# Performance work log

Hardware: AMD Instinct MI355X
Metric: run time of the kernel (lower is better)

Reference implementation:

```python
import jax, jax.numpy as jnp
import numpy as np

N = 20000          # nodes
E = 320000         # edges
G = 256            # g_dim
H1 = 256           # h1_dim (RGCN out)
H2 = 128           # h2_dim (per-head transformer out)
HEADS = 4
R = 8              # num relations
EPS_BN = 1e-5


def setup_inputs() -> dict:
    key = jax.random.key(0)
    ks = jax.random.split(key, 16)
    inp = {
        "node_features": jax.random.normal(ks[0], (N, G), jnp.float32),
        "node_type": jax.random.randint(ks[1], (N,), 0, 3),
        "edge_index": jax.random.randint(ks[2], (2, E), 0, N),
        "edge_type": jax.random.randint(ks[3], (E,), 0, R),
        # RGCNConv params
        "W_rel": jax.random.normal(ks[4], (R, G, H1), jnp.float32) * (1.0 / np.sqrt(G)),
        "W_root": jax.random.normal(ks[5], (G, H1), jnp.float32) * (1.0 / np.sqrt(G)),
        "b_rgcn": jnp.zeros((H1,), jnp.float32),
        # TransformerConv params (concat=True -> HEADS*H2 output)
        "W_q": jax.random.normal(ks[6], (H1, HEADS * H2), jnp.float32) * (1.0 / np.sqrt(H1)),
        "b_q": jnp.zeros((HEADS * H2,), jnp.float32),
        "W_k": jax.random.normal(ks[7], (H1, HEADS * H2), jnp.float32) * (1.0 / np.sqrt(H1)),
        "b_k": jnp.zeros((HEADS * H2,), jnp.float32),
        "W_v": jax.random.normal(ks[8], (H1, HEADS * H2), jnp.float32) * (1.0 / np.sqrt(H1)),
        "b_v": jnp.zeros((HEADS * H2,), jnp.float32),
        "W_skip": jax.random.normal(ks[9], (H1, HEADS * H2), jnp.float32) * (1.0 / np.sqrt(H1)),
        "b_skip": jnp.zeros((HEADS * H2,), jnp.float32),
        # BatchNorm1d params (training-mode batch stats)
        "bn_gamma": jnp.ones((HEADS * H2,), jnp.float32),
        "bn_beta": jnp.zeros((HEADS * H2,), jnp.float32),
    }
    return inp


def reference(node_features, node_type, edge_index, edge_type,
              W_rel, W_root, b_rgcn,
              W_q, b_q, W_k, b_k, W_v, b_v, W_skip, b_skip,
              bn_gamma, bn_beta):
    x = node_features
    src, dst = edge_index[0], edge_index[1]  # messages flow src -> dst

    # ---- RGCNConv (mean aggregation per relation, root weight, bias) ----
    xr = jnp.einsum('nd,rdh->nrh', x, W_rel)           # (N, R, H1)
    msg = xr[src, edge_type]                            # (E, H1)
    seg = dst * R + edge_type                           # combined (node, relation) segment id
    sums = jax.ops.segment_sum(msg, seg, num_segments=N * R)
    cnt = jax.ops.segment_sum(jnp.ones((E,), x.dtype), seg, num_segments=N * R)
    mean = sums / jnp.maximum(cnt, 1.0)[:, None]
    agg = mean.reshape(N, R, H1).sum(axis=1)            # sum over relations
    h1 = agg + x @ W_root + b_rgcn                      # (N, H1)

    # ---- TransformerConv (heads=HEADS, concat=True, root skip) ----
    q = (h1 @ W_q + b_q).reshape(N, HEADS, H2)
    k = (h1 @ W_k + b_k).reshape(N, HEADS, H2)
    v = (h1 @ W_v + b_v).reshape(N, HEADS, H2)

    scale = 1.0 / np.sqrt(H2)
    alpha = jnp.sum(q[dst] * k[src], axis=-1) * scale   # (E, HEADS)
    amax = jax.ops.segment_max(alpha, dst, num_segments=N)  # per-dst softmax max
    ea = jnp.exp(alpha - amax[dst])
    denom = jax.ops.segment_sum(ea, dst, num_segments=N)
    attn = ea / jnp.maximum(denom[dst], 1e-16)          # (E, HEADS)

    out = jax.ops.segment_sum(attn[:, :, None] * v[src], dst, num_segments=N)
    out = out.reshape(N, HEADS * H2) + h1 @ W_skip + b_skip

    # ---- BatchNorm1d (batch stats) + LeakyReLU(0.01) ----
    mu = out.mean(axis=0)
    var = out.var(axis=0)
    xn = (out - mu) * jax.lax.rsqrt(var + EPS_BN)
    y = bn_gamma * xn + bn_beta
    return jax.nn.leaky_relu(y, negative_slope=0.01)
```

## Files before the change

kernel.cpp:

```cpp
#include <hip/hip_runtime.h>

static const int N_NODES = 20000;
static const int N_EDGES = 320000;
static const int GDIM    = 256;
static const int H1DIM   = 256;
static const int C2DIM   = 512;
static const int NREL    = 8;
static const int NSEG    = N_NODES * NREL;

typedef _Float16 __attribute__((ext_vector_type(8))) half8;
typedef _Float16 __attribute__((ext_vector_type(4))) half4;
typedef _Float16 __attribute__((ext_vector_type(2))) half2v;
typedef __attribute__((ext_vector_type(4))) float f32x4;

__device__ __forceinline__ void gload_lds16(const void* g, void* l) {
  __builtin_amdgcn_global_load_lds(
      (const __attribute__((address_space(1))) unsigned int*)g,
      (__attribute__((address_space(3))) unsigned int*)l, 16, 0, 0);
}

__device__ __forceinline__ void swz_bxy(int& bx, int& by) {
  int nx   = gridDim.x;
  int nwg  = nx * gridDim.y;
  int orig = blockIdx.y * nx + blockIdx.x;
  int xcd  = orig & 7;
  int q    = nwg >> 3, r = nwg & 7;
  int base = xcd < r ? xcd * (q + 1) : r * (q + 1) + (xcd - r) * q;
  int wgid = base + (orig >> 3);
  bx = wgid % nx; by = wgid / nx;
}

template<int OUT_HALF>
__global__ __launch_bounds__(256) void gemm_mfma_k(
    const _Float16* __restrict__ A, const _Float16* __restrict__ Bt,
    const float* __restrict__ bias, void* __restrict__ Cout,
    int M, int N, int K)
{
  __shared__ _Float16 As[128 * 64];
  __shared__ _Float16 Bs[128 * 64];
  int bx, by; swz_bxy(bx, by);
  const int tid  = threadIdx.x;
  const int wid  = tid >> 6, lane = tid & 63;
  const int wr   = wid >> 1, wc = wid & 1;
  const int brow = by * 128;
  const int bcol = bx * 128;
  const int l15  = lane & 15, lhi = lane >> 4;
  const int srow = wid * 32;
  const int lrow = lane >> 3;
  const int lchk = lane & 7;

  f32x4 acc[4][4] = {};

  for (int k0 = 0; k0 < K; k0 += 64) {
    __syncthreads();
#pragma unroll
    for (int i = 0; i < 4; ++i) {
      int row = srow + i * 8 + lrow;
      int gc  = lchk ^ (row & 7);
      gload_lds16(A  + (size_t)(brow + row) * K + k0 + gc * 8,
                  &As[(srow + i * 8) * 64]);
      gload_lds16(Bt + (size_t)(bcol + row) * K + k0 + gc * 8,
                  &Bs[(srow + i * 8) * 64]);
    }
    __syncthreads();
#pragma unroll
    for (int kf = 0; kf < 2; ++kf) {
      int cc = kf * 4 + lhi;
      half8 af[4], bfr[4];
#pragma unroll
      for (int mi = 0; mi < 4; ++mi) {
        int row = wr * 64 + mi * 16 + l15;
        af[mi] = ((const half8*)As)[row * 8 + (cc ^ (row & 7))];
      }
#pragma unroll
      for (int ni = 0; ni < 4; ++ni) {
        int row = wc * 64 + ni * 16 + l15;
        bfr[ni] = ((const half8*)Bs)[row * 8 + (cc ^ (row & 7))];
      }
#pragma unroll
      for (int mi = 0; mi < 4; ++mi)
#pragma unroll
        for (int ni = 0; ni < 4; ++ni)
          acc[mi][ni] = __builtin_amdgcn_mfma_f32_16x16x32_f16(
              af[mi], bfr[ni], acc[mi][ni], 0, 0, 0);
    }
  }
#pragma unroll
  for (int ni = 0; ni < 4; ++ni) {
    int col = bcol + wc * 64 + ni * 16 + l15;
    float bb = bias ? bias[col] : 0.f;
#pragma unroll
    for (int mi = 0; mi < 4; ++mi) {
      int row0 = brow + wr * 64 + mi * 16 + lhi * 4;
#pragma unroll
      for (int j = 0; j < 4; ++j) {
        int r = row0 + j;
        if (r >= M) continue;
        float val = acc[mi][ni][j] + bb;
        if (OUT_HALF) ((_Float16*)Cout)[(size_t)r * N + col] = (_Float16)val;
        else          ((float*)Cout)[(size_t)r * N + col] = val;
      }
    }
  }
}

__global__ __launch_bounds__(256) void prep_k(
    const int* __restrict__ dst, const int* __restrict__ et, int* __restrict__ hist,
    const float* __restrict__ W_root, const float* __restrict__ W_rel,
    _Float16* __restrict__ Wt_cat2,
    const float* __restrict__ Wq, const float* __restrict__ Wk,
    const float* __restrict__ Wv, const float* __restrict__ Ws,
    const float* __restrict__ bq, const float* __restrict__ bk,
    const float* __restrict__ bv, const float* __restrict__ bs,
    _Float16* __restrict__ Wt_qk, float* __restrict__ bias_cat,
    const float* __restrict__ x, _Float16* __restrict__ xh)
{
  int b = blockIdx.x, tid = threadIdx.x;
  if (b < 1250) {
    int e = b * 256 + tid;
    if (e < N_EDGES) atomicAdd(&hist[dst[e] * NREL + et[e]], 1);
  } else if (b < 3554) {
    int idx = (b - 1250) * 256 + tid;
    int n2 = idx >> 8, k = idx & 255;
    float v;
    if (n2 < 256) v = W_root[(size_t)k * H1DIM + n2];
    else {
      int rr = (n2 - 256) >> 8, c = (n2 - 256) & 255;
      v = W_rel[((size_t)rr * 256 + k) * 256 + c];
    }
    Wt_cat2[idx] = (_Float16)v;
  } else if (b < 5602) {
    int idx = (b - 3554) * 256 + tid;
    int n = idx >> 8, k = idx & 255;
    int sel = n >> 9, c = n & 511;
    const float* W = sel == 0 ? Wq : sel == 1 ? Wk : sel == 2 ? Wv : Ws;
    Wt_qk[(size_t)n * 256 + k] = (_Float16)W[(size_t)k * C2DIM + c];
    if (k == 0) {
      const float* B = sel == 0 ? bq : sel == 1 ? bk : sel == 2 ? bv : bs;
      bias_cat[n] = B[c];
    }
  } else {
    int i = (b - 5602) * 256 + tid;
    float4 v = ((const float4*)x)[i];
    half4 o = {(_Float16)v.x, (_Float16)v.y, (_Float16)v.z, (_Float16)v.w};
    ((half4*)xh)[i] = o;
  }
}

__global__ __launch_bounds__(1024) void scan_local_k(
    const int* __restrict__ in, int* __restrict__ out, int* __restrict__ bsum, int n)
{
  __shared__ int s[1024];
  int gi = blockIdx.x * 1024 + threadIdx.x;
  int v = gi < n ? in[gi] : 0;
  s[threadIdx.x] = v; __syncthreads();
  for (int off = 1; off < 1024; off <<= 1) {
    int t = threadIdx.x >= off ? s[threadIdx.x - off] : 0;
    __syncthreads();
    s[threadIdx.x] += t;
    __syncthreads();
  }
  if (gi < n) out[gi] = s[threadIdx.x] - v;
  if (threadIdx.x == 1023) bsum[blockIdx.x] = s[1023];
}

__global__ __launch_bounds__(1024) void scan_addoff_k(
    int* __restrict__ off, const int* __restrict__ bsum,
    int* __restrict__ cur, int n, int nb)
{
  __shared__ int s[1024];
  int t = threadIdx.x;
  int v = t < nb ? bsum[t] : 0;
  s[t] = v; __syncthreads();
  for (int o = 1; o < 1024; o <<= 1) {
    int u = t >= o ? s[t - o] : 0;
    __syncthreads();
    s[t] += u;
    __syncthreads();
  }
  int blockOff = blockIdx.x == 0 ? 0 : s[blockIdx.x - 1];
  int gi = blockIdx.x * 1024 + t;
  if (gi < n) {
    int val = off[gi] + blockOff;
    off[gi] = val;
    cur[gi] = val;
  }
  if (gi == 0) off[n] = N_EDGES;
}

__global__ void reorder_k(const int* __restrict__ src, const int* __restrict__ dst,
                          const int* __restrict__ et,
                          int* __restrict__ cur, int* __restrict__ esrc)
{
  int e = blockIdx.x * blockDim.x + threadIdx.x;
  if (e >= N_EDGES) return;
  int seg = dst[e] * NREL + et[e];
  esrc[atomicAdd(&cur[seg], 1)] = src[e];
}

__global__ __launch_bounds__(256) void agg_h1_k(
    const _Float16* __restrict__ Y, const float* __restrict__ b_rgcn,
    const int* __restrict__ off, const int* __restrict__ esrc,
    _Float16* __restrict__ h1h)
{
  int d = blockIdx.x * 4 + (threadIdx.x >> 6);
  if (d >= N_NODES) return;
  int lane = threadIdx.x & 63;
  half4 rt = ((const half4*)(Y + (size_t)d * 2304))[lane];
  float4 bb = ((const float4*)b_rgcn)[lane];
  float4 acc = make_float4((float)rt.x + bb.x, (float)rt.y + bb.y,
                           (float)rt.z + bb.z, (float)rt.w + bb.w);
  for (int r = 0; r < NREL; ++r) {
    int seg = d * NREL + r;
    int beg = off[seg], end = off[seg + 1];
    if (beg >= end) continue;
    float4 a2 = make_float4(0.f, 0.f, 0.f, 0.f);
    for (int e = beg; e < end; ++e) {
      int s = esrc[e];
      half4 v = ((const half4*)(Y + (size_t)s * 2304 + 256 + r * 256))[lane];
      a2.x += (float)v.x; a2.y += (float)v.y;
      a2.z += (float)v.z; a2.w += (float)v.w;
    }
    float inv = 1.0f / (float)(end - beg);
    acc.x += a2.x * inv; acc.y += a2.y * inv;
    acc.z += a2.z * inv; acc.w += a2.w * inv;
  }
  half4 o = {(_Float16)acc.x, (_Float16)acc.y, (_Float16)acc.z, (_Float16)acc.w};
  ((half4*)(h1h + (size_t)d * 256))[lane] = o;
}

__global__ __launch_bounds__(256) void attn_fused_k(
    const _Float16* __restrict__ qkvs,
    const int* __restrict__ off, const int* __restrict__ esrc,
    _Float16* __restrict__ outh)
{
  int d = blockIdx.x * 4 + (threadIdx.x >> 6);
  if (d >= N_NODES) return;
  int lane = threadIdx.x & 63;
  half8 qr = ((const half8*)(qkvs + (size_t)d * 2048))[lane];
  float qf[8];
#pragma unroll
  for (int j = 0; j < 8; ++j) qf[j] = (float)qr[j];
  float m = -3.4e38f, ssum = 0.f;
  float av[8] = {};
  int beg = off[d * NREL], end = off[d * NREL + NREL];
  half8 krN = {}, vrN = {};
  if (beg < end) {
    int s0 = esrc[beg];
    const half8* row = (const half8*)(qkvs + (size_t)s0 * 2048 + 512);
    krN = row[lane];
    vrN = row[64 + lane];
  }
  for (int e = beg; e < end; ++e) {
    half8 kr = krN, vr = vrN;
    if (e + 1 < end) {
      int s1 = esrc[e + 1];
      const half8* row = (const half8*)(qkvs + (size_t)s1 * 2048 + 512);
      krN = row[lane];
      vrN = row[64 + lane];
    }
    float p = 0.f;
#pragma unroll
    for (int j = 0; j < 8; ++j) p += qf[j] * (float)kr[j];
    p += __shfl_xor(p, 1); p += __shfl_xor(p, 2);
    p += __shfl_xor(p, 4); p += __shfl_xor(p, 8);
    float a = p * 0.08838834764831845f;
    float mn = fmaxf(m, a);
    float corr = __expf(m - mn), w = __expf(a - mn);
    ssum = ssum * corr + w;
#pragma unroll
    for (int j = 0; j < 8; ++j) av[j] = av[j] * corr + w * (float)vr[j];
    m = mn;
  }
  float inv = 1.0f / fmaxf(ssum, 1e-16f);
  half8 sr = ((const half8*)(qkvs + (size_t)d * 2048 + 1536))[lane];
  half8 o;
#pragma unroll
  for (int j = 0; j < 8; ++j) o[j] = (_Float16)(av[j] * inv + (float)sr[j]);
  ((half8*)(outh + (size_t)d * C2DIM))[lane] = o;
}

__global__ __launch_bounds__(256) void bn_stats_k(
    const _Float16* __restrict__ x, float* __restrict__ sums, float* __restrict__ sumsq)
{
  int t = threadIdx.x;
  float s0 = 0.f, q0 = 0.f, s1 = 0.f, q1 = 0.f;
  for (int row = blockIdx.x; row < N_NODES; row += gridDim.x) {
    half2v v = ((const half2v*)(x + (size_t)row * C2DIM))[t];
    float a = (float)v.x, b = (float)v.y;
    s0 += a; q0 += a * a; s1 += b; q1 += b * b;
  }
  atomicAdd(&sums[2 * t], s0);  atomicAdd(&sums[2 * t + 1], s1);
  atomicAdd(&sumsq[2 * t], q0); atomicAdd(&sumsq[2 * t + 1], q1);
}

__global__ void bn_apply_k(const _Float16* __restrict__ xin, float* __restrict__ xout,
                           const float* __restrict__ sums, const float* __restrict__ sumsq,
                           const float* __restrict__ gamma, const float* __restrict__ beta,
                           int total8)
{
  int i = blockIdx.x * blockDim.x + threadIdx.x;
  if (i >= total8) return;
  int c0 = (i & 63) * 8;
  half8 v = ((const half8*)xin)[i];
  float o[8];
#pragma unroll
  for (int j = 0; j < 8; ++j) {
    int c = c0 + j;
    float mu  = sums[c] * (1.0f / N_NODES);
    float var = sumsq[c] * (1.0f / N_NODES) - mu * mu;
    float sc  = gamma[c] * rsqrtf(var + 1e-5f);
    float val = ((float)v[j] - mu) * sc + beta[c];
    o[j] = val >= 0.f ? val : 0.01f * val;
  }
  ((float4*)xout)[i * 2]     = make_float4(o[0], o[1], o[2], o[3]);
  ((float4*)xout)[i * 2 + 1] = make_float4(o[4], o[5], o[6], o[7]);
}

extern "C" void kernel_launch(void* const* d_in, const int* in_sizes, int n_in,
                              void* d_out, int out_size, void* d_ws, size_t ws_size,
                              hipStream_t stream)
{
  const float* x      = (const float*)d_in[0];
  const int*   ei     = (const int*)d_in[2];
  const int*   src    = ei;
  const int*   dst    = ei + N_EDGES;
  const int*   etype  = (const int*)d_in[3];
  const float* W_rel  = (const float*)d_in[4];
  const float* W_root = (const float*)d_in[5];
  const float* b_rgcn = (const float*)d_in[6];
  const float* W_q = (const float*)d_in[7];  const float* b_q = (const float*)d_in[8];
  const float* W_k = (const float*)d_in[9];  const float* b_k = (const float*)d_in[10];
  const float* W_v = (const float*)d_in[11]; const float* b_v = (const float*)d_in[12];
  const float* W_s = (const float*)d_in[13]; const float* b_s = (const float*)d_in[14];
  const float* gamma = (const float*)d_in[15];
  const float* beta  = (const float*)d_in[16];
  float* out = (float*)d_out;

  char* ws = (char*)d_ws;
  _Float16* Y      = (_Float16*)(ws + 0);
  _Float16* QKVS   = (_Float16*)(ws + 0);
  _Float16* outh   = (_Float16*)(ws + 81920000);
  _Float16* Wt_cat = (_Float16*)(ws + 92160000);
  _Float16* Wt_qk  = (_Float16*)(ws + 93339648);
  _Float16* h1h    = (_Float16*)(ws + 94388224);
  _Float16* xh     = h1h;

  char* C = ws + 104628224;
  int*   cur      = (int*)(C + 0);
  float* bns      = (float*)(C + 640000);
  float* bias_cat = (float*)(C + 648192);
  int*   off      = (int*)(C + 656384);
  int*   esrc     = (int*)(C + 1296400);
  int*   bsum     = (int*)(C + 2576400);
  float* bnsum = bns, *bnsq = bns + 512;

  hipMemsetAsync(C, 0, 648192, stream);

  dim3 blk(256);
  const int NB = (NSEG + 1023) / 1024;

  prep_k<<<dim3(10602), blk, 0, stream>>>(
      dst, etype, cur,
      W_root, W_rel, Wt_cat,
      W_q, W_k, W_v, W_s, b_q, b_k, b_v, b_s, Wt_qk, bias_cat,
      x, xh);

  scan_local_k<<<dim3(NB), dim3(1024), 0, stream>>>(cur, off, bsum, NSEG);
  scan_addoff_k<<<dim3(NB), dim3(1024), 0, stream>>>(off, bsum, cur, NSEG, NB);
  reorder_k<<<dim3((N_EDGES + 255) / 256), blk, 0, stream>>>(
      src, dst, etype, cur, esrc);

  gemm_mfma_k<1><<<dim3(2304 / 128, (N_NODES + 127) / 128), blk, 0, stream>>>(
      xh, Wt_cat, nullptr, Y, N_NODES, 2304, 256);

  agg_h1_k<<<dim3((N_NODES + 3) / 4), blk, 0, stream>>>(Y, b_rgcn, off, esrc, h1h);

  gemm_mfma_k<1><<<dim3(2048 / 128, (N_NODES + 127) / 128), blk, 0, stream>>>(
      h1h, Wt_qk, bias_cat, QKVS, N_NODES, 2048, 256);

  attn_fused_k<<<dim3((N_NODES + 3) / 4), blk, 0, stream>>>(QKVS, off, esrc, outh);

  bn_stats_k<<<dim3(208), blk, 0, stream>>>(outh, bnsum, bnsq);
  bn_apply_k<<<dim3((N_NODES * C2DIM / 8 + 255) / 256), blk, 0, stream>>>(
      outh, out, bnsum, bnsq, gamma, beta, N_NODES * C2DIM / 8);
}
```

Measured before the change: 369.7 us.

## Aggregate raw features per relation before transform, then run one wide-K RGCN GEMM

The RGCN layer is reordered from transform-then-aggregate to aggregate-then-transform. Previously a GEMM produced per-relation transformed features for every node (N×2304 outputs), which were then gathered and averaged per destination. Now the per-relation means are taken over the small half-precision input rows and written into a concatenated [x | mean_r] matrix. A single GEMM with K=2304 and 256 outputs then produces h1 with the bias folded in, and the weight prep is rewritten to build the matching transposed layout. The gathers now hit a much smaller source array with better cache locality, at the cost of a large intermediate write and a narrow-N GEMM with fewer output tiles.

```diff
diff --git a/kernel.cpp b/kernel.cpp
--- a/kernel.cpp
+++ b/kernel.cpp
@@ -107,7 +107,7 @@
 __global__ __launch_bounds__(256) void prep_k(
     const int* __restrict__ dst, const int* __restrict__ et, int* __restrict__ hist,
     const float* __restrict__ W_root, const float* __restrict__ W_rel,
-    _Float16* __restrict__ Wt_cat2,
+    _Float16* __restrict__ Wt_cat,
     const float* __restrict__ Wq, const float* __restrict__ Wk,
     const float* __restrict__ Wv, const float* __restrict__ Ws,
     const float* __restrict__ bq, const float* __restrict__ bk,
@@ -121,14 +121,10 @@
     if (e < N_EDGES) atomicAdd(&hist[dst[e] * NREL + et[e]], 1);
   } else if (b < 3554) {
     int idx = (b - 1250) * 256 + tid;
-    int n2 = idx >> 8, k = idx & 255;
-    float v;
-    if (n2 < 256) v = W_root[(size_t)k * H1DIM + n2];
-    else {
-      int rr = (n2 - 256) >> 8, c = (n2 - 256) & 255;
-      v = W_rel[((size_t)rr * 256 + k) * 256 + c];
-    }
-    Wt_cat2[idx] = (_Float16)v;
+    int n = idx / 2304, k = idx % 2304;
+    float v = (k < 256) ? W_root[(size_t)k * H1DIM + n]
+                        : W_rel[(size_t)(k - 256) * H1DIM + n];
+    Wt_cat[idx] = (_Float16)v;
   } else if (b < 5602) {
     int idx = (b - 3554) * 256 + tid;
     int n = idx >> 8, k = idx & 255;
@@ -198,35 +194,32 @@
   esrc[atomicAdd(&cur[seg], 1)] = src[e];
 }
 
-__global__ __launch_bounds__(256) void agg_h1_k(
-    const _Float16* __restrict__ Y, const float* __restrict__ b_rgcn,
-    const int* __restrict__ off, const int* __restrict__ esrc,
-    _Float16* __restrict__ h1h)
+__global__ __launch_bounds__(256) void agg_xcat_k(
+    const _Float16* __restrict__ xh, const int* __restrict__ off,
+    const int* __restrict__ esrc, _Float16* __restrict__ Xcat)
 {
   int d = blockIdx.x * 4 + (threadIdx.x >> 6);
   if (d >= N_NODES) return;
   int lane = threadIdx.x & 63;
-  half4 rt = ((const half4*)(Y + (size_t)d * 2304))[lane];
-  float4 bb = ((const float4*)b_rgcn)[lane];
-  float4 acc = make_float4((float)rt.x + bb.x, (float)rt.y + bb.y,
-                           (float)rt.z + bb.z, (float)rt.w + bb.w);
+  _Float16* xrow = Xcat + (size_t)d * 2304;
+  half4 xv = ((const half4*)(xh + (size_t)d * GDIM))[lane];
+  *(half4*)(xrow + lane * 4) = xv;
   for (int r = 0; r < NREL; ++r) {
     int seg = d * NREL + r;
     int beg = off[seg], end = off[seg + 1];
-    if (beg >= end) continue;
-    float4 a2 = make_float4(0.f, 0.f, 0.f, 0.f);
+    float4 acc = make_float4(0.f, 0.f, 0.f, 0.f);
     for (int e = beg; e < end; ++e) {
       int s = esrc[e];
-      half4 v = ((const half4*)(Y + (size_t)s * 2304 + 256 + r * 256))[lane];
-      a2.x += (float)v.x; a2.y += (float)v.y;
-      a2.z += (float)v.z; a2.w += (float)v.w;
-    }
-    float inv = 1.0f / (float)(end - beg);
-    acc.x += a2.x * inv; acc.y += a2.y * inv;
-    acc.z += a2.z * inv; acc.w += a2.w * inv;
-  }
-  half4 o = {(_Float16)acc.x, (_Float16)acc.y, (_Float16)acc.z, (_Float16)acc.w};
-  ((half4*)(h1h + (size_t)d * 256))[lane] = o;
+      half4 v = ((const half4*)(xh + (size_t)s * GDIM))[lane];
+      acc.x += (float)v.x; acc.y += (float)v.y;
+      acc.z += (float)v.z; acc.w += (float)v.w;
+    }
+    float inv = (end > beg) ? 1.0f / (float)(end - beg) : 0.0f;
+    half4 o;
+    o.x = (_Float16)(acc.x * inv); o.y = (_Float16)(acc.y * inv);
+    o.z = (_Float16)(acc.z * inv); o.w = (_Float16)(acc.w * inv);
+    *(half4*)(xrow + 256 + r * 256 + lane * 4) = o;
+  }
 }
 
 __global__ __launch_bounds__(256) void attn_fused_k(
@@ -338,7 +331,7 @@
   float* out = (float*)d_out;
 
   char* ws = (char*)d_ws;
-  _Float16* Y      = (_Float16*)(ws + 0);
+  _Float16* Xcat   = (_Float16*)(ws + 0);
   _Float16* QKVS   = (_Float16*)(ws + 0);
   _Float16* outh   = (_Float16*)(ws + 81920000);
   _Float16* Wt_cat = (_Float16*)(ws + 92160000);
@@ -371,10 +364,10 @@
   reorder_k<<<dim3((N_EDGES + 255) / 256), blk, 0, stream>>>(
       src, dst, etype, cur, esrc);
 
-  gemm_mfma_k<1><<<dim3(2304 / 128, (N_NODES + 127) / 128), blk, 0, stream>>>(
-      xh, Wt_cat, nullptr, Y, N_NODES, 2304, 256);
-
-  agg_h1_k<<<dim3((N_NODES + 3) / 4), blk, 0, stream>>>(Y, b_rgcn, off, esrc, h1h);
+  agg_xcat_k<<<dim3((N_NODES + 3) / 4), blk, 0, stream>>>(xh, off, esrc, Xcat);
+
+  gemm_mfma_k<1><<<dim3(H1DIM / 128, (N_NODES + 127) / 128), blk, 0, stream>>>(
+      Xcat, Wt_cat, b_rgcn, h1h, N_NODES, H1DIM, 2304);
 
   gemm_mfma_k<1><<<dim3(2048 / 128, (N_NODES + 127) / 128), blk, 0, stream>>>(
       h1h, Wt_qk, bias_cat, QKVS, N_NODES, 2048, 256);
```

New measurement: 358.4 us. 1.03x faster.
